# Optimization experiments

Measured on AMD Instinct MI355X. Metric: run time of the kernel, lower is better.

Reference implementation:

```python
import jax, jax.numpy as jnp
import numpy as np

B, T, N, F_IN, F_OUT, K = 16, 12, 1024, 64, 64, 3


def setup_inputs() -> dict:
    key = jax.random.key(0)
    k1, k2, k3, k4 = jax.random.split(key, 4)
    x = jax.random.normal(k1, (B, T, N, F_IN), dtype=jnp.float32)
    spatial_attention = jax.random.uniform(k2, (B, N, N), dtype=jnp.float32)
    cheb = jax.random.normal(k3, (K, N, N), dtype=jnp.float32) / np.sqrt(N)
    # Xavier-uniform-ish init for Theta [K, F_in, F_out]
    limit = np.sqrt(6.0 / (F_IN + F_OUT))
    Theta = jax.random.uniform(k4, (K, F_IN, F_OUT), dtype=jnp.float32,
                               minval=-limit, maxval=limit)
    return {"x": x, "spatial_attention": spatial_attention, "cheb": cheb, "Theta": Theta}


def reference(x, spatial_attention, cheb, Theta):
    # Attention-weighted Chebyshev adjacencies: [B, K, N, N]
    A = cheb[None, :, :, :] * spatial_attention[:, None, :, :]
    # Graph propagation for all t, k at once: [B, T, K, N, F_in]
    rhs = jnp.einsum('bkij,btjf->btkif', A, x)
    # Per-order linear map + sum over K: [B, T, N, F_out]
    out = jnp.einsum('btkif,kfo->btio', rhs, Theta)
    return jax.nn.relu(out)
```

## Files before the change

### kernel.cpp

```cpp
#include <hip/hip_runtime.h>
#include <hip/hip_bf16.h>

#define BB 16
#define TT 12
#define NN 1024
#define FF 64
#define KC 3

typedef __bf16 bf16x8 __attribute__((ext_vector_type(8)));
typedef float  f32x4  __attribute__((ext_vector_type(4)));
typedef float  f32x16 __attribute__((ext_vector_type(16)));

#define A_TILE 24576
#define X_TILE 32768

#define MFMA_B(a, b, c) __builtin_amdgcn_mfma_f32_32x32x16_bf16(a, b, c, 0, 0, 0)

__global__ __launch_bounds__(512, 2) void cheb_fused(
    const float* __restrict__ x,
    const float* __restrict__ att,
    const float* __restrict__ cheb,
    const float* __restrict__ Theta,
    float* __restrict__ out)
{
    __shared__ __align__(16) char lds_raw[2 * (A_TILE + X_TILE)];
    char* Ab0 = lds_raw;
    char* Xb0 = lds_raw + A_TILE;
    char* Ab1 = lds_raw + A_TILE + X_TILE;
    char* Xb1 = Ab1 + A_TILE;

    const int tid  = threadIdx.x;
    const int lane = tid & 63;
    const int wid  = tid >> 6;

    const int wg = (blockIdx.x & 7) * 96 + (blockIdx.x >> 3);
    const int b  = wg / 48;
    const int it = (wg % 48) / 3;
    const int tc = wg % 3;
    const int i_base = it * 64;
    const int t_base = tc * 4;

    const int wm  = wid >> 1;
    const int wn  = wid & 1;
    const int l31 = lane & 31;
    const int lg  = lane >> 5;
    const int sw3 = (l31 >> 2) & 7;

    const float* attB = att + (size_t)b * NN * NN;
    const float* xB   = x + (size_t)b * TT * NN * FF;

    const int r_a = tid >> 3;
    const int g_a = tid & 7;
    const int swza_st = ((r_a >> 2) & 7) << 4;
    int tl_s[4], jj_s[4], f_s[4], swzx_st[4];
    #pragma unroll
    for (int s = 0; s < 4; ++s) {
        int u   = tid + s * 512;
        tl_s[s] = u >> 9;
        int rem = u & 511;
        jj_s[s] = (rem >> 4) * 2;
        f_s[s]  = (rem & 15) * 4;
        swzx_st[s] = ((f_s[s] >> 2) & 7) << 4;
    }

    f32x4 ra0, ra1, rc0[KC], rc1[KC], rx0[4], rx1[4];

    auto load_tile = [&](int j0) {
        const float* ap = attB + (size_t)(i_base + r_a) * NN + j0 + g_a * 8;
        ra0 = *reinterpret_cast<const f32x4*>(ap);
        ra1 = *reinterpret_cast<const f32x4*>(ap + 4);
        #pragma unroll
        for (int k = 0; k < KC; ++k) {
            const float* cp = cheb + ((size_t)k * NN + i_base + r_a) * NN + j0 + g_a * 8;
            rc0[k] = *reinterpret_cast<const f32x4*>(cp);
            rc1[k] = *reinterpret_cast<const f32x4*>(cp + 4);
        }
        #pragma unroll
        for (int s = 0; s < 4; ++s) {
            const float* xp = xB + ((size_t)(t_base + tl_s[s]) * NN + j0 + jj_s[s]) * FF + f_s[s];
            rx0[s] = *reinterpret_cast<const f32x4*>(xp);
            rx1[s] = *reinterpret_cast<const f32x4*>(xp + FF);
        }
    };

    auto store_A = [&](char* Ab) {
        #pragma unroll
        for (int k = 0; k < KC; ++k) {
            bf16x8 w;
            #pragma unroll
            for (int e = 0; e < 4; ++e) {
                w[e]     = (__bf16)(rc0[k][e] * ra0[e]);
                w[e + 4] = (__bf16)(rc1[k][e] * ra1[e]);
            }
            *reinterpret_cast<bf16x8*>(Ab + (k * 64 + r_a) * 128 + ((g_a * 16) ^ swza_st)) = w;
        }
    };

    auto store_X = [&](char* Xb) {
        #pragma unroll
        for (int s = 0; s < 4; ++s) {
            const int c0     = tl_s[s] * 64 + f_s[s];
            const int coloff = (jj_s[s] * 2) ^ swzx_st[s];
            #pragma unroll
            for (int e = 0; e < 4; ++e) {
                union { __bf16 h[2]; unsigned u32; } pk;
                pk.h[0] = (__bf16)rx0[s][e];
                pk.h[1] = (__bf16)rx1[s][e];
                *reinterpret_cast<unsigned*>(Xb + (c0 + e) * 128 + coloff) = pk.u32;
            }
        }
    };

    f32x16 acc[KC][2] = {};
    const int xrow0 = (wm * 64 + l31) * 128;
    const int xrow1 = xrow0 + 32 * 128;
    const int arow  = (wn * 32 + l31) * 128;

    auto phase = [&](const char* AbR, const char* XbR, int kk) {
        const int off = ((kk * 2 + lg) ^ sw3) << 4;
        bf16x8 af0 = *reinterpret_cast<const bf16x8*>(XbR + xrow0 + off);
        bf16x8 af1 = *reinterpret_cast<const bf16x8*>(XbR + xrow1 + off);
        bf16x8 b0  = *reinterpret_cast<const bf16x8*>(AbR + arow + off);
        bf16x8 b1  = *reinterpret_cast<const bf16x8*>(AbR + 8192 + arow + off);
        bf16x8 b2  = *reinterpret_cast<const bf16x8*>(AbR + 16384 + arow + off);
        __builtin_amdgcn_s_setprio(1);
        acc[0][0] = MFMA_B(af0, b0, acc[0][0]); acc[0][1] = MFMA_B(af1, b0, acc[0][1]);
        acc[1][0] = MFMA_B(af0, b1, acc[1][0]); acc[1][1] = MFMA_B(af1, b1, acc[1][1]);
        acc[2][0] = MFMA_B(af0, b2, acc[2][0]); acc[2][1] = MFMA_B(af1, b2, acc[2][1]);
        __builtin_amdgcn_s_setprio(0);
    };

    load_tile(0);
    store_A(Ab0);
    store_X(Xb0);
    load_tile(64);
    asm volatile("s_waitcnt lgkmcnt(0)" ::: "memory");
    __builtin_amdgcn_s_barrier();

    for (int jt2 = 0; jt2 < 8; ++jt2) {
        const int jt = jt2 * 2;
        phase(Ab0, Xb0, 0);
        phase(Ab0, Xb0, 1);
        store_A(Ab1);
        phase(Ab0, Xb0, 2);
        store_X(Xb1);
        phase(Ab0, Xb0, 3);
        if (jt + 2 < 16) load_tile((jt + 2) * 64);
        asm volatile("s_waitcnt lgkmcnt(0)" ::: "memory");
        __builtin_amdgcn_s_barrier();

        phase(Ab1, Xb1, 0);
        phase(Ab1, Xb1, 1);
        if (jt + 1 < 15) store_A(Ab0);
        phase(Ab1, Xb1, 2);
        if (jt + 1 < 15) store_X(Xb0);
        phase(Ab1, Xb1, 3);
        if (jt + 3 < 16) load_tile((jt + 3) * 64);
        asm volatile("s_waitcnt lgkmcnt(0)" ::: "memory");
        __builtin_amdgcn_s_barrier();
    }

    {
        const int fi0 = wid * 3;
        #pragma unroll
        for (int q = 0; q < 3; ++q) {
            int fi = fi0 + q;
            int k  = fi >> 3;
            int mo = (fi >> 2) & 1;
            int s  = fi & 3;
            int o  = 32 * mo + l31;
            int fb = 32 * (s >> 1) + 16 * (s & 1) + 4 * lg;
            bf16x8 v;
            #pragma unroll
            for (int e = 0; e < 8; ++e) {
                int f = fb + (e & 3) + 8 * (e >> 2);
                v[e] = (__bf16)Theta[(k * FF + f) * FF + o];
            }
            *reinterpret_cast<bf16x8*>(lds_raw + (fi * 64 + lane) * 16) = v;
        }
    }
    __syncthreads();

    f32x16 of[2] = {};
    #pragma unroll
    for (int k = 0; k < KC; ++k) {
        #pragma unroll
        for (int s = 0; s < 4; ++s) {
            bf16x8 pb;
            #pragma unroll
            for (int e = 0; e < 8; ++e)
                pb[e] = (__bf16)acc[k][s >> 1][e + 8 * (s & 1)];
            #pragma unroll
            for (int mo = 0; mo < 2; ++mo) {
                bf16x8 th = *reinterpret_cast<const bf16x8*>(
                    lds_raw + ((((k * 2 + mo) * 4 + s) * 64) + lane) * 16);
                of[mo] = MFMA_B(pb, th, of[mo]);
            }
        }
    }

    const int t = t_base + wm;
    float* op = out + (((size_t)b * TT + t) * NN + i_base + wn * 32) * FF;
    #pragma unroll
    for (int mo = 0; mo < 2; ++mo) {
        #pragma unroll
        for (int r = 0; r < 16; ++r) {
            int row = (r & 3) + 8 * (r >> 2) + 4 * lg;
            int o   = 32 * mo + l31;
            float v = of[mo][r];
            op[(size_t)row * FF + o] = v > 0.0f ? v : 0.0f;
        }
    }
}

extern "C" void kernel_launch(void* const* d_in, const int* in_sizes, int n_in,
                              void* d_out, int out_size, void* d_ws, size_t ws_size,
                              hipStream_t stream) {
    const float* x     = (const float*)d_in[0];
    const float* att   = (const float*)d_in[1];
    const float* cheb  = (const float*)d_in[2];
    const float* Theta = (const float*)d_in[3];
    float* out = (float*)d_out;
    (void)d_ws; (void)ws_size; (void)in_sizes; (void)n_in; (void)out_size;

    dim3 grid(BB * (NN / 64) * (TT / 4));
    cheb_fused<<<grid, 512, 0, stream>>>(x, att, cheb, Theta, out);
}
```

Baseline: 127.1 us.

## Pre-pack x into bf16 MFMA fragments and cheb to bf16 before main GEMM

Adds two pre-pass kernels. One converts x into bf16 fragments already laid out for the MFMA operand in workspace; the other converts cheb to bf16. A new main kernel with 256 threads per block and 2 timesteps per block then reads the x fragments straight from global memory, so the X tile no longer goes through LDS, and it halves the cheb bytes it loads. The LDS double buffer now holds only the attention-weighted A tile, and the loop is restructured to one sync per tile. The price is extra launches and a round trip of about 31 MB through the workspace, plus attention being re-read by twice as many blocks. The old fused kernel is kept as a fallback when the workspace is too small.

After: 157.9 us. 1.24x slower.

```diff
diff --git a/kernel.cpp b/kernel.cpp
--- a/kernel.cpp
+++ b/kernel.cpp
@@ -7,64 +7,274 @@
 #define FF 64
 #define KC 3
 
-typedef __bf16 bf16x8 __attribute__((ext_vector_type(8)));
-typedef float  f32x4  __attribute__((ext_vector_type(4)));
-typedef float  f32x16 __attribute__((ext_vector_type(16)));
+typedef __bf16  bf16x8 __attribute__((ext_vector_type(8)));
+typedef float   f32x4  __attribute__((ext_vector_type(4)));
+typedef float   f32x16 __attribute__((ext_vector_type(16)));
+typedef unsigned short u16;
 
 #define A_TILE 24576
-#define X_TILE 32768
-
 #define MFMA_B(a, b, c) __builtin_amdgcn_mfma_f32_32x32x16_bf16(a, b, c, 0, 0, 0)
 
-__global__ __launch_bounds__(512, 2) void cheb_fused(
-    const float* __restrict__ x,
+#define YF_BYTES 25165824ull
+#define CB_BYTES 6291456ull
+
+static __device__ __forceinline__ u16 f2bf(float v) {
+    union { __bf16 b; u16 u; } c; c.b = (__bf16)v; return c.u;
+}
+
+__global__ __launch_bounds__(256) void x_to_yfrags(
+    const float* __restrict__ x, u16* __restrict__ y)
+{
+    __shared__ char tl[64 * 128];
+    const int tid = threadIdx.x;
+    const int bt  = blockIdx.x >> 4;
+    const int jt  = blockIdx.x & 15;
+    const int f   = tid & 63;
+    const int jr  = tid >> 6;
+
+    const float* xp = x + ((size_t)bt * NN + jt * 64 + jr) * FF + f;
+    #pragma unroll
+    for (int stp = 0; stp < 16; ++stp) {
+        int j = stp * 4 + jr;
+        u16 h = f2bf(xp[stp * 4 * FF]);
+        *reinterpret_cast<u16*>(tl + j * 128 + ((f * 2) ^ ((j & 7) << 4))) = h;
+    }
+    __syncthreads();
+
+    u16* yo = y + ((size_t)bt * 16 + jt) * 4096;
+    #pragma unroll
+    for (int p = 0; p < 2; ++p) {
+        int c  = tid + p * 256;
+        int s  = c >> 6, fo = c & 63;
+        int j0 = (s >> 1) * 16 + (s & 1) * 8;
+        u16 h[8];
+        #pragma unroll
+        for (int e = 0; e < 8; ++e)
+            h[e] = *reinterpret_cast<u16*>(tl + (j0 + e) * 128 + ((fo * 2) ^ (e << 4)));
+        uint4 w;
+        w.x = h[0] | ((unsigned)h[1] << 16);
+        w.y = h[2] | ((unsigned)h[3] << 16);
+        w.z = h[4] | ((unsigned)h[5] << 16);
+        w.w = h[6] | ((unsigned)h[7] << 16);
+        *reinterpret_cast<uint4*>(yo + (size_t)c * 8) = w;
+    }
+}
+
+__global__ __launch_bounds__(256) void cheb_to_bf16(
+    const float* __restrict__ c, u16* __restrict__ o)
+{
+    const size_t i = ((size_t)blockIdx.x * 256 + threadIdx.x) * 8;
+    f32x4 a = *reinterpret_cast<const f32x4*>(c + i);
+    f32x4 b = *reinterpret_cast<const f32x4*>(c + i + 4);
+    u16 h[8];
+    #pragma unroll
+    for (int e = 0; e < 4; ++e) { h[e] = f2bf(a[e]); h[e + 4] = f2bf(b[e]); }
+    uint4 w;
+    w.x = h[0] | ((unsigned)h[1] << 16);
+    w.y = h[2] | ((unsigned)h[3] << 16);
+    w.z = h[4] | ((unsigned)h[5] << 16);
+    w.w = h[6] | ((unsigned)h[7] << 16);
+    *reinterpret_cast<uint4*>(o + i) = w;
+}
+
+__global__ __launch_bounds__(256, 3) void cheb_main(
+    const u16*  __restrict__ yfr,
     const float* __restrict__ att,
-    const float* __restrict__ cheb,
+    const u16*  __restrict__ chb,
     const float* __restrict__ Theta,
     float* __restrict__ out)
 {
-    __shared__ __align__(16) char lds_raw[2 * (A_TILE + X_TILE)];
-    char* Ab0 = lds_raw;
-    char* Xb0 = lds_raw + A_TILE;
-    char* Ab1 = lds_raw + A_TILE + X_TILE;
-    char* Xb1 = Ab1 + A_TILE;
+    __shared__ __align__(16) char lds[2 * A_TILE];
+    char* Ab0 = lds;
+    char* Ab1 = lds + A_TILE;
 
     const int tid  = threadIdx.x;
     const int lane = tid & 63;
     const int wid  = tid >> 6;
 
+    const int wg = (blockIdx.x & 7) * 192 + (blockIdx.x >> 3);
+    const int b  = wg / 96;
+    const int rm = wg % 96;
+    const int it = rm / 6;
+    const int tc = rm % 6;
+    const int i_base = it * 64;
+    const int t_base = tc * 2;
+
+    const int wm  = wid >> 1;
+    const int wn  = wid & 1;
+    const int l31 = lane & 31;
+    const int lg  = lane >> 5;
+    const int sw3 = (l31 >> 2) & 7;
+
+    const int rr = tid >> 2;
+    const int g2 = tid & 3;
+    const int swz_st = ((rr >> 2) & 7) << 4;
+    const float* attR = att + ((size_t)b * NN + i_base + rr) * NN + g2 * 16;
+    const u16*   chR  = chb + ((size_t)(i_base + rr)) * NN + g2 * 16;
+
+    const u16* yt0 = yfr + ((size_t)(b * TT + t_base + wm) * 16) * 4096
+                   + (size_t)(lg * 512 + l31 * 8);
+
+    f32x16 acc[KC][2] = {};
+    const int arow = (wn * 32 + l31) * 128;
+
+    f32x4 ra[4];
+    bf16x8 rc[KC][2];
+
+    auto LOADS = [&](int j0) {
+        #pragma unroll
+        for (int q = 0; q < 4; ++q)
+            ra[q] = *reinterpret_cast<const f32x4*>(attR + j0 + q * 4);
+        #pragma unroll
+        for (int k = 0; k < KC; ++k) {
+            const u16* cp = chR + (size_t)k * NN * NN + j0;
+            rc[k][0] = *reinterpret_cast<const bf16x8*>(cp);
+            rc[k][1] = *reinterpret_cast<const bf16x8*>(cp + 8);
+        }
+    };
+    auto FINISH = [&](char* Ab) {
+        #pragma unroll
+        for (int k = 0; k < KC; ++k) {
+            #pragma unroll
+            for (int h = 0; h < 2; ++h) {
+                bf16x8 w;
+                #pragma unroll
+                for (int e = 0; e < 8; ++e) {
+                    float av = ra[(h * 8 + e) >> 2][(h * 8 + e) & 3];
+                    w[e] = (__bf16)(av * (float)rc[k][h][e]);
+                }
+                *reinterpret_cast<bf16x8*>(
+                    Ab + (k * 64 + rr) * 128 + (((g2 * 2 + h) * 16) ^ swz_st)) = w;
+            }
+        }
+    };
+
+    auto phase = [&](const char* AbR, const u16* yt, int kk) {
+        const int off = ((kk * 2 + lg) ^ sw3) << 4;
+        const u16* yp = yt + kk * 2 * 512;
+        bf16x8 af0 = *reinterpret_cast<const bf16x8*>(yp);
+        bf16x8 af1 = *reinterpret_cast<const bf16x8*>(yp + 256);
+        bf16x8 b0  = *reinterpret_cast<const bf16x8*>(AbR + arow + off);
+        bf16x8 b1  = *reinterpret_cast<const bf16x8*>(AbR + 8192 + arow + off);
+        bf16x8 b2  = *reinterpret_cast<const bf16x8*>(AbR + 16384 + arow + off);
+        __builtin_amdgcn_s_setprio(1);
+        acc[0][0] = MFMA_B(af0, b0, acc[0][0]); acc[0][1] = MFMA_B(af1, b0, acc[0][1]);
+        acc[1][0] = MFMA_B(af0, b1, acc[1][0]); acc[1][1] = MFMA_B(af1, b1, acc[1][1]);
+        acc[2][0] = MFMA_B(af0, b2, acc[2][0]); acc[2][1] = MFMA_B(af1, b2, acc[2][1]);
+        __builtin_amdgcn_s_setprio(0);
+    };
+
+    LOADS(0);
+    FINISH(Ab0);
+    __syncthreads();
+
+    for (int jt = 0; jt < 16; ++jt) {
+        char* cur = (jt & 1) ? Ab1 : Ab0;
+        char* alt = (jt & 1) ? Ab0 : Ab1;
+        if (jt < 15) LOADS((jt + 1) * 64);
+        const u16* yt = yt0 + (size_t)jt * 4096;
+        phase(cur, yt, 0);
+        phase(cur, yt, 1);
+        phase(cur, yt, 2);
+        phase(cur, yt, 3);
+        if (jt < 15) FINISH(alt);
+        __syncthreads();
+    }
+
+    {
+        const int fi0 = wid * 6;
+        #pragma unroll
+        for (int q = 0; q < 6; ++q) {
+            int fi = fi0 + q;
+            int k  = fi >> 3;
+            int mo = (fi >> 2) & 1;
+            int s  = fi & 3;
+            int o  = 32 * mo + l31;
+            int fb = 32 * (s >> 1) + 16 * (s & 1) + 4 * lg;
+            bf16x8 v;
+            #pragma unroll
+            for (int e = 0; e < 8; ++e) {
+                int f = fb + (e & 3) + 8 * (e >> 2);
+                v[e] = (__bf16)Theta[(k * FF + f) * FF + o];
+            }
+            *reinterpret_cast<bf16x8*>(lds + (fi * 64 + lane) * 16) = v;
+        }
+    }
+    __syncthreads();
+
+    f32x16 of[2] = {};
+    #pragma unroll
+    for (int k = 0; k < KC; ++k) {
+        #pragma unroll
+        for (int s = 0; s < 4; ++s) {
+            bf16x8 pb;
+            #pragma unroll
+            for (int e = 0; e < 8; ++e)
+                pb[e] = (__bf16)acc[k][s >> 1][e + 8 * (s & 1)];
+            #pragma unroll
+            for (int mo = 0; mo < 2; ++mo) {
+                bf16x8 th = *reinterpret_cast<const bf16x8*>(
+                    lds + ((((k * 2 + mo) * 4 + s) * 64) + lane) * 16);
+                of[mo] = MFMA_B(pb, th, of[mo]);
+            }
+        }
+    }
+
+    const int t = t_base + wm;
+    float* op = out + (((size_t)b * TT + t) * NN + i_base + wn * 32) * FF;
+    #pragma unroll
+    for (int mo = 0; mo < 2; ++mo) {
+        #pragma unroll
+        for (int r = 0; r < 16; ++r) {
+            int row = (r & 3) + 8 * (r >> 2) + 4 * lg;
+            int o   = 32 * mo + l31;
+            float v = of[mo][r];
+            op[(size_t)row * FF + o] = v > 0.0f ? v : 0.0f;
+        }
+    }
+}
+
+__global__ __launch_bounds__(512, 2) void cheb_fused(
+    const float* __restrict__ x, const float* __restrict__ att,
+    const float* __restrict__ cheb, const float* __restrict__ Theta,
+    float* __restrict__ out)
+{
+    __shared__ __align__(16) char lds_raw[2 * (A_TILE + 32768)];
+    char* Ab0 = lds_raw;
+    char* Xb0 = lds_raw + A_TILE;
+    char* Ab1 = lds_raw + A_TILE + 32768;
+    char* Xb1 = Ab1 + A_TILE;
+
+    const int tid  = threadIdx.x;
+    const int lane = tid & 63;
+    const int wid  = tid >> 6;
     const int wg = (blockIdx.x & 7) * 96 + (blockIdx.x >> 3);
     const int b  = wg / 48;
     const int it = (wg % 48) / 3;
     const int tc = wg % 3;
     const int i_base = it * 64;
     const int t_base = tc * 4;
-
     const int wm  = wid >> 1;
     const int wn  = wid & 1;
     const int l31 = lane & 31;
     const int lg  = lane >> 5;
     const int sw3 = (l31 >> 2) & 7;
-
     const float* attB = att + (size_t)b * NN * NN;
     const float* xB   = x + (size_t)b * TT * NN * FF;
-
     const int r_a = tid >> 3;
     const int g_a = tid & 7;
     const int swza_st = ((r_a >> 2) & 7) << 4;
     int tl_s[4], jj_s[4], f_s[4], swzx_st[4];
     #pragma unroll
     for (int s = 0; s < 4; ++s) {
-        int u   = tid + s * 512;
+        int u = tid + s * 512;
         tl_s[s] = u >> 9;
         int rem = u & 511;
         jj_s[s] = (rem >> 4) * 2;
         f_s[s]  = (rem & 15) * 4;
         swzx_st[s] = ((f_s[s] >> 2) & 7) << 4;
     }
-
     f32x4 ra0, ra1, rc0[KC], rc1[KC], rx0[4], rx1[4];
-
     auto load_tile = [&](int j0) {
         const float* ap = attB + (size_t)(i_base + r_a) * NN + j0 + g_a * 8;
         ra0 = *reinterpret_cast<const f32x4*>(ap);
@@ -82,7 +292,6 @@
             rx1[s] = *reinterpret_cast<const f32x4*>(xp + FF);
         }
     };
-
     auto store_A = [&](char* Ab) {
         #pragma unroll
         for (int k = 0; k < KC; ++k) {
@@ -95,11 +304,10 @@
             *reinterpret_cast<bf16x8*>(Ab + (k * 64 + r_a) * 128 + ((g_a * 16) ^ swza_st)) = w;
         }
     };
-
     auto store_X = [&](char* Xb) {
         #pragma unroll
         for (int s = 0; s < 4; ++s) {
-            const int c0     = tl_s[s] * 64 + f_s[s];
+            const int c0 = tl_s[s] * 64 + f_s[s];
             const int coloff = (jj_s[s] * 2) ^ swzx_st[s];
             #pragma unroll
             for (int e = 0; e < 4; ++e) {
@@ -110,12 +318,10 @@
             }
         }
     };
-
     f32x16 acc[KC][2] = {};
     const int xrow0 = (wm * 64 + l31) * 128;
     const int xrow1 = xrow0 + 32 * 128;
     const int arow  = (wn * 32 + l31) * 128;
-
     auto phase = [&](const char* AbR, const char* XbR, int kk) {
         const int off = ((kk * 2 + lg) ^ sw3) << 4;
         bf16x8 af0 = *reinterpret_cast<const bf16x8*>(XbR + xrow0 + off);
@@ -129,14 +335,12 @@
         acc[2][0] = MFMA_B(af0, b2, acc[2][0]); acc[2][1] = MFMA_B(af1, b2, acc[2][1]);
         __builtin_amdgcn_s_setprio(0);
     };
-
     load_tile(0);
     store_A(Ab0);
     store_X(Xb0);
     load_tile(64);
     asm volatile("s_waitcnt lgkmcnt(0)" ::: "memory");
     __builtin_amdgcn_s_barrier();
-
     for (int jt2 = 0; jt2 < 8; ++jt2) {
         const int jt = jt2 * 2;
         phase(Ab0, Xb0, 0);
@@ -148,7 +352,6 @@
         if (jt + 2 < 16) load_tile((jt + 2) * 64);
         asm volatile("s_waitcnt lgkmcnt(0)" ::: "memory");
         __builtin_amdgcn_s_barrier();
-
         phase(Ab1, Xb1, 0);
         phase(Ab1, Xb1, 1);
         if (jt + 1 < 15) store_A(Ab0);
@@ -159,7 +362,6 @@
         asm volatile("s_waitcnt lgkmcnt(0)" ::: "memory");
         __builtin_amdgcn_s_barrier();
     }
-
     {
         const int fi0 = wid * 3;
         #pragma unroll
@@ -180,7 +382,6 @@
         }
     }
     __syncthreads();
-
     f32x16 of[2] = {};
     #pragma unroll
     for (int k = 0; k < KC; ++k) {
@@ -198,7 +399,6 @@
             }
         }
     }
-
     const int t = t_base + wm;
     float* op = out + (((size_t)b * TT + t) * NN + i_base + wn * 32) * FF;
     #pragma unroll
@@ -221,8 +421,15 @@
     const float* cheb  = (const float*)d_in[2];
     const float* Theta = (const float*)d_in[3];
     float* out = (float*)d_out;
-    (void)d_ws; (void)ws_size; (void)in_sizes; (void)n_in; (void)out_size;
-
-    dim3 grid(BB * (NN / 64) * (TT / 4));
-    cheb_fused<<<grid, 512, 0, stream>>>(x, att, cheb, Theta, out);
-}
+    (void)in_sizes; (void)n_in; (void)out_size;
+
+    if (ws_size >= YF_BYTES + CB_BYTES) {
+        u16* yfr = (u16*)d_ws;
+        u16* cbf = (u16*)((char*)d_ws + YF_BYTES);
+        x_to_yfrags<<<dim3(BB * TT * 16), 256, 0, stream>>>(x, yfr);
+        cheb_to_bf16<<<dim3(KC * NN * NN / (256 * 8)), 256, 0, stream>>>(cheb, cbf);
+        cheb_main<<<dim3(BB * 16 * 6), 256, 0, stream>>>(yfr, att, cbf, Theta, out);
+    } else {
+        cheb_fused<<<dim3(BB * 16 * 3), 512, 0, stream>>>(x, att, cheb, Theta, out);
+    }
+}
```
